# Kernel optimization log

Measured on AMD Instinct MI355X. Metric: run time of the kernel, lower is better.

## Reference

```python
import jax, jax.numpy as jnp
import numpy as np

NUM_GROUPS = 32
NUM_HEADS = 8
EPS = 1e-5


def setup_inputs() -> dict:
    key = jax.random.key(0)
    ks = jax.random.split(key, 3)
    C = 512
    x = jax.random.normal(ks[0], (4, C, 48, 48), dtype=jnp.float32)
    gamma = jnp.ones((C,), jnp.float32)
    beta = jnp.zeros((C,), jnp.float32)
    w_qkv = jax.random.normal(ks[1], (C, 3 * C), jnp.float32) * (1.0 / np.sqrt(C))
    b_qkv = jnp.zeros((3 * C,), jnp.float32)
    w_proj = jax.random.normal(ks[2], (C, C), jnp.float32) * (1.0 / np.sqrt(C))
    b_proj = jnp.zeros((C,), jnp.float32)
    return {"x": x, "gamma": gamma, "beta": beta, "w_qkv": w_qkv,
            "b_qkv": b_qkv, "w_proj": w_proj, "b_proj": b_proj}


def group_norm(x, gamma, beta):
    # x: (b, c, h, w); 32 groups over channel dim
    b, c, h, w = x.shape
    xg = x.reshape(b, NUM_GROUPS, c // NUM_GROUPS, h, w)
    mu = jnp.mean(xg, axis=(2, 3, 4), keepdims=True)
    var = jnp.var(xg, axis=(2, 3, 4), keepdims=True)
    xn = ((xg - mu) * jax.lax.rsqrt(var + EPS)).reshape(b, c, h, w)
    return xn * gamma[None, :, None, None] + beta[None, :, None, None]


def reference(x, gamma, beta, w_qkv, b_qkv, w_proj, b_proj):
    b, c, h, w = x.shape
    hd = c // NUM_HEADS
    scale = hd ** -0.5
    xn = group_norm(x, gamma, beta)
    x_flat = xn.reshape(b, c, h * w).transpose(0, 2, 1)          # (b, s, c)
    qkv = x_flat @ w_qkv + b_qkv                                  # (b, s, 3c)
    q, k, v = jnp.split(qkv, 3, axis=-1)
    s = h * w
    # (b, heads, s, hd)
    q = q.reshape(b, s, NUM_HEADS, hd).transpose(0, 2, 1, 3)
    k = k.reshape(b, s, NUM_HEADS, hd).transpose(0, 2, 1, 3)
    v = v.reshape(b, s, NUM_HEADS, hd).transpose(0, 2, 1, 3)
    attn = jnp.einsum('bhqd,bhkd->bhqk', q, k) * scale            # (b, h, s, s)
    attn = jax.nn.softmax(attn, axis=-1)
    out = jnp.einsum('bhqk,bhkd->bhqd', attn, v)                  # (b, h, s, hd)
    out = out.transpose(0, 2, 1, 3).reshape(b, s, c)
    out = out @ w_proj + b_proj                                   # (b, s, c)
    return x + out.transpose(0, 2, 1).reshape(b, c, h, w)
```

## Files before the change

kernel.cpp:

```cpp
#include <hip/hip_runtime.h>
#include <hip/hip_bf16.h>
#include <stdint.h>

#define S_LEN 2304
#define C_DIM 512
#define NH 8
#define HD 64

typedef __attribute__((ext_vector_type(8))) __bf16 bf16x8;
typedef __attribute__((ext_vector_type(4))) float f32x4;
typedef __attribute__((ext_vector_type(16))) float f32x16;
typedef __attribute__((ext_vector_type(8))) unsigned short u16x8;
typedef __attribute__((ext_vector_type(4))) unsigned short u16x4;

__device__ __forceinline__ unsigned short bf16u(float f) {
  __hip_bfloat16 h = __float2bfloat16(f);
  return __builtin_bit_cast(unsigned short, h);
}

__device__ __forceinline__ void load_lds16(const void* g, void* l) {
  __builtin_amdgcn_global_load_lds(
      (const __attribute__((address_space(1))) void*)g,
      (__attribute__((address_space(3))) void*)l, 16, 0, 0);
}

__global__ __launch_bounds__(256) void gn_stats_kernel(const float* __restrict__ x,
                                                       float* __restrict__ stats) {
  const int bg = blockIdx.x;
  const float4* src = (const float4*)(x + (size_t)bg * 36864);
  float s = 0.f, s2 = 0.f;
#pragma unroll
  for (int i = 0; i < 36; ++i) {
    float4 v = src[i * 256 + threadIdx.x];
    s += v.x + v.y + v.z + v.w;
    s2 += v.x * v.x + v.y * v.y + v.z * v.z + v.w * v.w;
  }
#pragma unroll
  for (int off = 1; off < 64; off <<= 1) {
    s += __shfl_xor(s, off);
    s2 += __shfl_xor(s2, off);
  }
  __shared__ float red[8];
  const int wid = threadIdx.x >> 6;
  if ((threadIdx.x & 63) == 0) { red[wid] = s; red[wid + 4] = s2; }
  __syncthreads();
  if (threadIdx.x == 0) {
    float S = red[0] + red[1] + red[2] + red[3];
    float S2 = red[4] + red[5] + red[6] + red[7];
    float mu = S * (1.f / 36864.f);
    float var = S2 * (1.f / 36864.f) - mu * mu;
    stats[bg * 2] = mu;
    stats[bg * 2 + 1] = rsqrtf(var + 1e-5f);
  }
}

__global__ __launch_bounds__(256) void gn_norm_t_kernel(
    const float* __restrict__ x, const float* __restrict__ gamma,
    const float* __restrict__ beta, const float* __restrict__ stats,
    unsigned short* __restrict__ xn) {
  __shared__ float tile[64][68];
  const int s0 = blockIdx.x * 64, c0 = blockIdx.y * 64, b = blockIdx.z;
  const int tid = threadIdx.x;
  {
    const int cl = tid >> 2, sc = (tid & 3) * 16;
    const float* src = x + ((size_t)b * C_DIM + c0 + cl) * S_LEN + s0 + sc;
#pragma unroll
    for (int i = 0; i < 4; ++i)
      *(float4*)&tile[cl][sc + i * 4] = *(const float4*)(src + i * 4);
  }
  __syncthreads();
  const int sl = tid >> 2, cc = (tid & 3) * 16;
  const int g = (c0 + cc) >> 4;
  const float mu = stats[((size_t)b * 32 + g) * 2];
  const float rs = stats[((size_t)b * 32 + g) * 2 + 1];
  u16x8 o0, o1;
#pragma unroll
  for (int j = 0; j < 8; ++j) {
    const int c = c0 + cc + j;
    o0[j] = bf16u((tile[cc + j][sl] - mu) * rs * gamma[c] + beta[c]);
  }
#pragma unroll
  for (int j = 0; j < 8; ++j) {
    const int c = c0 + cc + 8 + j;
    o1[j] = bf16u((tile[cc + 8 + j][sl] - mu) * rs * gamma[c] + beta[c]);
  }
  unsigned short* dst = xn + ((size_t)b * S_LEN + s0 + sl) * C_DIM + c0 + cc;
  *(u16x8*)dst = o0;
  *(u16x8*)(dst + 8) = o1;
}

__global__ __launch_bounds__(256) void wt_kernel(const float* __restrict__ w,
                                                 unsigned short* __restrict__ wT,
                                                 int N, int K) {
  __shared__ float tile[64][68];
  const int n0 = blockIdx.x * 64, k0 = blockIdx.y * 64;
  const int tid = threadIdx.x;
  {
    const int kl = tid >> 2, nc = (tid & 3) * 16;
    const float* src = w + (size_t)(k0 + kl) * N + n0 + nc;
#pragma unroll
    for (int i = 0; i < 4; ++i)
      *(float4*)&tile[kl][nc + i * 4] = *(const float4*)(src + i * 4);
  }
  __syncthreads();
  const int nl = tid >> 2, kc = (tid & 3) * 16;
  u16x8 o0, o1;
#pragma unroll
  for (int j = 0; j < 8; ++j) o0[j] = bf16u(tile[kc + j][nl]);
#pragma unroll
  for (int j = 0; j < 8; ++j) o1[j] = bf16u(tile[kc + 8 + j][nl]);
  unsigned short* dst = wT + (size_t)(n0 + nl) * K + k0 + kc;
  *(u16x8*)dst = o0;
  *(u16x8*)(dst + 8) = o1;
}

__device__ __forceinline__ void gemm128_core(const unsigned short* __restrict__ A,
                                             const unsigned short* __restrict__ B,
                                             int K, int m0, int n0, short* lds_a,
                                             short* lds_b, f32x4 (&acc)[4][4]) {
  const int tid = threadIdx.x;
  const int lane = tid & 63, wid = tid >> 6;
  const int wr = wid >> 1, wc = wid & 1;
  const f32x4 fzero = {0.f, 0.f, 0.f, 0.f};
#pragma unroll
  for (int i = 0; i < 4; ++i)
#pragma unroll
    for (int j = 0; j < 4; ++j) acc[i][j] = fzero;
  const int lrow = lane >> 3;
  const int lcol = (lane & 7) * 8;
  for (int kt = 0; kt < K; kt += 64) {
#pragma unroll
    for (int i = 0; i < 4; ++i) {
      const int r0 = (wid * 4 + i) * 8;
      load_lds16((const void*)(A + (size_t)(m0 + r0 + lrow) * K + kt + lcol), lds_a + r0 * 64);
      load_lds16((const void*)(B + (size_t)(n0 + r0 + lrow) * K + kt + lcol), lds_b + r0 * 64);
    }
    __syncthreads();
#pragma unroll
    for (int ks = 0; ks < 2; ++ks) {
      bf16x8 af[4], bfr[4];
#pragma unroll
      for (int mf = 0; mf < 4; ++mf)
        af[mf] = *(const bf16x8*)(lds_a + ((wr * 64 + mf * 16 + (lane & 15)) * 64 +
                                           ks * 32 + (lane >> 4) * 8));
#pragma unroll
      for (int nf = 0; nf < 4; ++nf)
        bfr[nf] = *(const bf16x8*)(lds_b + ((wc * 64 + nf * 16 + (lane & 15)) * 64 +
                                            ks * 32 + (lane >> 4) * 8));
#pragma unroll
      for (int mf = 0; mf < 4; ++mf)
#pragma unroll
        for (int nf = 0; nf < 4; ++nf)
          acc[mf][nf] =
              __builtin_amdgcn_mfma_f32_16x16x32_bf16(af[mf], bfr[nf], acc[mf][nf], 0, 0, 0);
    }
    __syncthreads();
  }
}

__global__ __launch_bounds__(256) void qkv_gemm_kernel(
    const unsigned short* __restrict__ xn, const unsigned short* __restrict__ wT,
    const float* __restrict__ bq, unsigned short* __restrict__ Qb,
    unsigned short* __restrict__ Kb, unsigned short* __restrict__ Vt) {
  __shared__ short lds_a[128 * 64];
  __shared__ short lds_b[128 * 64];
  const int b = blockIdx.z;
  const int m0 = blockIdx.x * 128, n0 = blockIdx.y * 128;
  f32x4 acc[4][4];
  gemm128_core(xn + (size_t)b * S_LEN * C_DIM, wT, C_DIM, m0, n0, lds_a, lds_b, acc);
  const int lane = threadIdx.x & 63, wid = threadIdx.x >> 6;
  const int wr = wid >> 1, wc = wid & 1;
#pragma unroll
  for (int mf = 0; mf < 4; ++mf) {
#pragma unroll
    for (int nf = 0; nf < 4; ++nf) {
      const int n = n0 + wc * 64 + nf * 16 + (lane & 15);
      const int part = n >> 9;
      const int h = (n >> 6) & 7;
      const int d = n & 63;
      const float bias = bq[n];
      const int m = m0 + wr * 64 + mf * 16 + (lane >> 4) * 4;
      if (part == 2) {
        u16x4 pk;
#pragma unroll
        for (int r = 0; r < 4; ++r) pk[r] = bf16u(acc[mf][nf][r] + bias);
        *(u16x4*)(Vt + ((size_t)(b * NH + h) * HD + d) * S_LEN + m) = pk;
      } else {
        unsigned short* dst = part == 0 ? Qb : Kb;
        const float sc = part == 0 ? 0.18033688011112042f : 1.0f;
#pragma unroll
        for (int r = 0; r < 4; ++r)
          dst[((size_t)(b * NH + h) * S_LEN + m + r) * HD + d] =
              bf16u((acc[mf][nf][r] + bias) * sc);
      }
    }
  }
}

#define QBLK 96
__global__ __launch_bounds__(192) void attn_kernel(const unsigned short* __restrict__ Q,
                                                   const unsigned short* __restrict__ K,
                                                   const unsigned short* __restrict__ Vt,
                                                   unsigned short* __restrict__ O) {
  __shared__ __align__(16) char smem[45056];
  const int tid = threadIdx.x;
  const int w = tid >> 6, l = tid & 63;
  const int l31 = l & 31, hi = l >> 5;
  const int bh = blockIdx.y, b = bh >> 3, h = bh & 7;
  const int q0 = blockIdx.x * QBLK;

  const char* gQ = (const char*)Q + (size_t)bh * S_LEN * 128;
  const char* gK = (const char*)K + (size_t)bh * S_LEN * 128;
  const char* gV = (const char*)Vt + (size_t)bh * HD * (S_LEN * 2);

  const char* kvp[6];
  unsigned kvadv[6];
  bool kvok[6];
#pragma unroll
  for (int i = 0; i < 6; ++i) {
    const int c = i * 192 + tid;
    kvok[i] = (c < 1024);
    if (c < 512) {
      const int r = c >> 3, ch = c & 7;
      kvp[i] = gK + (size_t)r * 128 + ((ch ^ (r & 7)) << 4);
      kvadv[i] = 64 * 128;
    } else {
      const int c2 = c & 511;
      const int dd = c2 >> 3, ch = c2 & 7;
      kvp[i] = gV + (size_t)dd * (S_LEN * 2) + ((ch ^ (dd & 7)) << 4);
      kvadv[i] = 128;
    }
  }

  auto stage_kv = [&](char* nreg) {
#pragma unroll
    for (int i = 0; i < 6; ++i) {
      if (kvok[i]) {
        load_lds16((const void*)kvp[i], nreg + (i * 192 + w * 64) * 16);
        kvp[i] += kvadv[i];
      }
    }
  };

#pragma unroll
  for (int i = 0; i < 4; ++i) {
    const int c0 = i * 192 + w * 64;
    const int c = c0 + l;
    const int r = c >> 3, ch = c & 7;
    load_lds16((const void*)(gQ + (size_t)(q0 + r) * 128 + ((ch ^ (r & 7)) << 4)),
               smem + c0 * 16);
  }
  stage_kv(smem + 12288);
  if (w == 0) asm volatile("s_waitcnt vmcnt(6)" ::: "memory");
  else        asm volatile("s_waitcnt vmcnt(5)" ::: "memory");
  __builtin_amdgcn_s_barrier();

  bf16x8 qf[4];
  {
    const int qrow = w * 32 + l31;
    const int qsw = qrow & 7;
#pragma unroll
    for (int d4 = 0; d4 < 4; ++d4)
      qf[d4] = *(const bf16x8*)(smem + qrow * 128 + (((d4 * 2 + hi) ^ qsw) << 4));
  }

  float m_run = -1e30f, lsum = 0.f;
  f32x16 oac0, oac1;
#pragma unroll
  for (int i = 0; i < 16; ++i) { oac0[i] = 0.f; oac1[i] = 0.f; }

  for (int kt = 0; kt < 36; ++kt) {
    char* region = smem + 12288 + ((kt & 1) << 14);
    if (kt < 35) {
      stage_kv(smem + 12288 + (((kt + 1) & 1) << 14));
      if (w == 0) asm volatile("s_waitcnt vmcnt(6)" ::: "memory");
      else        asm volatile("s_waitcnt vmcnt(5)" ::: "memory");
    } else {
      asm volatile("s_waitcnt vmcnt(0)" ::: "memory");
    }
    __builtin_amdgcn_s_barrier();

    const char* kreg = region;
    const char* vreg = region + 8192;
#pragma unroll
    for (int sub = 0; sub < 2; ++sub) {
      f32x16 st;
#pragma unroll
      for (int i = 0; i < 16; ++i) st[i] = 0.f;
      const int krow = sub * 32 + l31;
      const int ksw = krow & 7;
#pragma unroll
      for (int d4 = 0; d4 < 4; ++d4) {
        bf16x8 kf = *(const bf16x8*)(kreg + krow * 128 + (((d4 * 2 + hi) ^ ksw) << 4));
        st = __builtin_amdgcn_mfma_f32_32x32x16_bf16(kf, qf[d4], st, 0, 0, 0);
      }
      float t8[8];
#pragma unroll
      for (int i = 0; i < 8; ++i) t8[i] = fmaxf(st[2 * i], st[2 * i + 1]);
#pragma unroll
      for (int i = 0; i < 4; ++i) t8[i] = fmaxf(t8[i], t8[i + 4]);
      float mt = fmaxf(fmaxf(t8[0], t8[1]), fmaxf(t8[2], t8[3]));
      float mo = mt;
      asm volatile("v_permlane32_swap_b32 %0, %1" : "+v"(mt), "+v"(mo));
      mt = fmaxf(mt, mo);
      const float mnew = fmaxf(m_run, mt);
      if (__any((mt - m_run) > 8.f)) {
        const float corr = exp2f(m_run - mnew);
#pragma unroll
        for (int i = 0; i < 16; ++i) { oac0[i] *= corr; oac1[i] *= corr; }
        lsum *= corr;
        m_run = mnew;
      }
      float p[16];
#pragma unroll
      for (int i = 0; i < 16; ++i) p[i] = exp2f(st[i] - m_run);
      float a8[8];
#pragma unroll
      for (int i = 0; i < 8; ++i) a8[i] = p[2 * i] + p[2 * i + 1];
#pragma unroll
      for (int i = 0; i < 4; ++i) a8[i] += a8[i + 4];
      float rs = (a8[0] + a8[1]) + (a8[2] + a8[3]);
      float rsc = rs;
      asm volatile("v_permlane32_swap_b32 %0, %1" : "+v"(rs), "+v"(rsc));
      lsum += rs + rsc;
      unsigned int wv[8];
#pragma unroll
      for (int j = 0; j < 8; ++j)
        asm("v_cvt_pk_bf16_f32 %0, %1, %2" : "=v"(wv[j]) : "v"(p[2 * j]), "v"(p[2 * j + 1]));
      asm volatile("v_permlane32_swap_b32 %0, %1" : "+v"(wv[0]), "+v"(wv[2]));
      asm volatile("v_permlane32_swap_b32 %0, %1" : "+v"(wv[1]), "+v"(wv[3]));
      asm volatile("v_permlane32_swap_b32 %0, %1" : "+v"(wv[4]), "+v"(wv[6]));
      asm volatile("v_permlane32_swap_b32 %0, %1" : "+v"(wv[5]), "+v"(wv[7]));
      typedef __attribute__((ext_vector_type(4))) unsigned int u32x4;
      u32x4 pw0 = {wv[0], wv[1], wv[2], wv[3]};
      u32x4 pw1 = {wv[4], wv[5], wv[6], wv[7]};
      bf16x8 pf0 = __builtin_bit_cast(bf16x8, pw0);
      bf16x8 pf1 = __builtin_bit_cast(bf16x8, pw1);
      {
        const int vrow = l31;
        const int vsw = vrow & 7;
        bf16x8 vf0 = *(const bf16x8*)(vreg + vrow * 128 + (((sub * 4 + 0 + hi) ^ vsw) << 4));
        oac0 = __builtin_amdgcn_mfma_f32_32x32x16_bf16(vf0, pf0, oac0, 0, 0, 0);
        bf16x8 vf1 = *(const bf16x8*)(vreg + vrow * 128 + (((sub * 4 + 2 + hi) ^ vsw) << 4));
        oac0 = __builtin_amdgcn_mfma_f32_32x32x16_bf16(vf1, pf1, oac0, 0, 0, 0);
      }
      {
        const int vrow = 32 + l31;
        const int vsw = vrow & 7;
        bf16x8 vf0 = *(const bf16x8*)(vreg + vrow * 128 + (((sub * 4 + 0 + hi) ^ vsw) << 4));
        oac1 = __builtin_amdgcn_mfma_f32_32x32x16_bf16(vf0, pf0, oac1, 0, 0, 0);
        bf16x8 vf1 = *(const bf16x8*)(vreg + vrow * 128 + (((sub * 4 + 2 + hi) ^ vsw) << 4));
        oac1 = __builtin_amdgcn_mfma_f32_32x32x16_bf16(vf1, pf1, oac1, 0, 0, 0);
      }
    }
    __builtin_amdgcn_s_barrier();
  }

  __syncthreads();
  const float inv = 1.f / lsum;
  unsigned short* ob = (unsigned short*)smem;
  const int qrow = w * 32 + l31;
#pragma unroll
  for (int g = 0; g < 4; ++g) {
    u16x4 pk;
#pragma unroll
    for (int r = 0; r < 4; ++r) pk[r] = bf16u(oac0[g * 4 + r] * inv);
    *(u16x4*)(ob + qrow * 72 + (g * 8 + hi * 4)) = pk;
  }
#pragma unroll
  for (int g = 0; g < 4; ++g) {
    u16x4 pk;
#pragma unroll
    for (int r = 0; r < 4; ++r) pk[r] = bf16u(oac1[g * 4 + r] * inv);
    *(u16x4*)(ob + qrow * 72 + (32 + g * 8 + hi * 4)) = pk;
  }
  __syncthreads();
#pragma unroll
  for (int i = 0; i < 4; ++i) {
    const int c = i * 192 + tid;
    const int row = c >> 3, c8 = (c & 7) * 8;
    u16x8 v = *(const u16x8*)(ob + row * 72 + c8);
    *(u16x8*)(O + ((size_t)b * S_LEN + q0 + row) * C_DIM + h * HD + c8) = v;
  }
}

__global__ __launch_bounds__(256) void proj_gemm_kernel(
    const unsigned short* __restrict__ wT, const unsigned short* __restrict__ ao,
    const float* __restrict__ bp, const float* __restrict__ x, float* __restrict__ out) {
  __shared__ short lds_a[128 * 64];
  __shared__ short lds_b[128 * 64];
  const int b = blockIdx.z;
  const int m0 = blockIdx.x * 128, n0 = blockIdx.y * 128;
  f32x4 acc[4][4];
  gemm128_core(wT, ao + (size_t)b * S_LEN * C_DIM, C_DIM, m0, n0, lds_a, lds_b, acc);
  const int lane = threadIdx.x & 63, wid = threadIdx.x >> 6;
  const int wr = wid >> 1, wc = wid & 1;
#pragma unroll
  for (int mf = 0; mf < 4; ++mf) {
#pragma unroll
    for (int nf = 0; nf < 4; ++nf) {
      const int n = n0 + wc * 64 + nf * 16 + (lane & 15);
#pragma unroll
      for (int r = 0; r < 4; ++r) {
        const int m = m0 + wr * 64 + mf * 16 + (lane >> 4) * 4 + r;
        const size_t idx = ((size_t)b * C_DIM + m) * S_LEN + n;
        out[idx] = x[idx] + acc[mf][nf][r] + bp[m];
      }
    }
  }
}

extern "C" void kernel_launch(void* const* d_in, const int* in_sizes, int n_in,
                              void* d_out, int out_size, void* d_ws, size_t ws_size,
                              hipStream_t stream) {
  const float* x = (const float*)d_in[0];
  const float* gamma = (const float*)d_in[1];
  const float* beta = (const float*)d_in[2];
  const float* w_qkv = (const float*)d_in[3];
  const float* b_qkv = (const float*)d_in[4];
  const float* w_proj = (const float*)d_in[5];
  const float* b_proj = (const float*)d_in[6];
  float* out = (float*)d_out;

  char* ws = (char*)d_ws;
  float* stats = (float*)ws;
  unsigned short* xn = (unsigned short*)(ws + 1024);
  unsigned short* wqkvT = (unsigned short*)(ws + 9438208);
  unsigned short* wprojT = (unsigned short*)(ws + 11011072);
  unsigned short* Qb = (unsigned short*)(ws + 11535360);
  unsigned short* Kb = (unsigned short*)(ws + 20972544);
  unsigned short* Vt = (unsigned short*)(ws + 30409728);
  unsigned short* ao = (unsigned short*)(ws + 39846912);

  hipLaunchKernelGGL(gn_stats_kernel, dim3(128), dim3(256), 0, stream, x, stats);
  hipLaunchKernelGGL(wt_kernel, dim3(24, 8), dim3(256), 0, stream, w_qkv, wqkvT, 3 * C_DIM, C_DIM);
  hipLaunchKernelGGL(wt_kernel, dim3(8, 8), dim3(256), 0, stream, w_proj, wprojT, C_DIM, C_DIM);
  hipLaunchKernelGGL(gn_norm_t_kernel, dim3(36, 8, 4), dim3(256), 0, stream, x, gamma, beta, stats, xn);
  hipLaunchKernelGGL(qkv_gemm_kernel, dim3(18, 12, 4), dim3(256), 0, stream, xn, wqkvT, b_qkv, Qb, Kb, Vt);
  hipLaunchKernelGGL(attn_kernel, dim3(24, 32), dim3(192), 0, stream, Qb, Kb, Vt, ao);
  hipLaunchKernelGGL(proj_gemm_kernel, dim3(4, 18, 4), dim3(256), 0, stream, wprojT, ao, b_proj, x, out);
}
```

Baseline: 179.3 us.

## Triple-buffer K/V staging, load Q to registers, compute row sums with MFMA

New measurement: 194.3 us. 8.4% more time.

```diff
diff --git a/kernel.cpp b/kernel.cpp
--- a/kernel.cpp
+++ b/kernel.cpp
@@ -12,6 +12,7 @@
 typedef __attribute__((ext_vector_type(16))) float f32x16;
 typedef __attribute__((ext_vector_type(8))) unsigned short u16x8;
 typedef __attribute__((ext_vector_type(4))) unsigned short u16x4;
+typedef __attribute__((ext_vector_type(4))) unsigned int u32x4;
 
 __device__ __forceinline__ unsigned short bf16u(float f) {
   __hip_bfloat16 h = __float2bfloat16(f);
@@ -22,6 +23,12 @@
   __builtin_amdgcn_global_load_lds(
       (const __attribute__((address_space(1))) void*)g,
       (__attribute__((address_space(3))) void*)l, 16, 0, 0);
+}
+
+__device__ __forceinline__ float max3f(float a, float b, float c) {
+  float d;
+  asm("v_max3_f32 %0, %1, %2, %3" : "=v"(d) : "v"(a), "v"(b), "v"(c));
+  return d;
 }
 
 __global__ __launch_bounds__(256) void gn_stats_kernel(const float* __restrict__ x,
@@ -202,7 +209,7 @@
                                                    const unsigned short* __restrict__ K,
                                                    const unsigned short* __restrict__ Vt,
                                                    unsigned short* __restrict__ O) {
-  __shared__ __align__(16) char smem[45056];
+  __shared__ __align__(16) char smem[49152];
   const int tid = threadIdx.x;
   const int w = tid >> 6, l = tid & 63;
   const int l31 = l & 31, hi = l >> 5;
@@ -212,6 +219,14 @@
   const char* gQ = (const char*)Q + (size_t)bh * S_LEN * 128;
   const char* gK = (const char*)K + (size_t)bh * S_LEN * 128;
   const char* gV = (const char*)Vt + (size_t)bh * HD * (S_LEN * 2);
+
+  bf16x8 qf[4];
+  {
+    const char* qp = gQ + (size_t)(q0 + w * 32 + l31) * 128 + hi * 16;
+#pragma unroll
+    for (int d4 = 0; d4 < 4; ++d4) qf[d4] = *(const bf16x8*)(qp + d4 * 32);
+  }
+  asm volatile("" : "+v"(qf[0]), "+v"(qf[1]), "+v"(qf[2]), "+v"(qf[3]));
 
   const char* kvp[6];
   unsigned kvadv[6];
@@ -242,37 +257,26 @@
     }
   };
 
-#pragma unroll
-  for (int i = 0; i < 4; ++i) {
-    const int c0 = i * 192 + w * 64;
-    const int c = c0 + l;
-    const int r = c >> 3, ch = c & 7;
-    load_lds16((const void*)(gQ + (size_t)(q0 + r) * 128 + ((ch ^ (r & 7)) << 4)),
-               smem + c0 * 16);
-  }
-  stage_kv(smem + 12288);
-  if (w == 0) asm volatile("s_waitcnt vmcnt(6)" ::: "memory");
-  else        asm volatile("s_waitcnt vmcnt(5)" ::: "memory");
-  __builtin_amdgcn_s_barrier();
-
-  bf16x8 qf[4];
-  {
-    const int qrow = w * 32 + l31;
-    const int qsw = qrow & 7;
-#pragma unroll
-    for (int d4 = 0; d4 < 4; ++d4)
-      qf[d4] = *(const bf16x8*)(smem + qrow * 128 + (((d4 * 2 + hi) ^ qsw) << 4));
-  }
-
-  float m_run = -1e30f, lsum = 0.f;
-  f32x16 oac0, oac1;
-#pragma unroll
-  for (int i = 0; i < 16; ++i) { oac0[i] = 0.f; oac1[i] = 0.f; }
-
+  stage_kv(smem);
+  stage_kv(smem + 16384);
+
+  const u16x8 onesu = {0x3F80, 0x3F80, 0x3F80, 0x3F80, 0x3F80, 0x3F80, 0x3F80, 0x3F80};
+  const bf16x8 onesf = __builtin_bit_cast(bf16x8, onesu);
+
+  float m_run = -1e30f;
+  f32x16 oac0, oac1, lacc;
+#pragma unroll
+  for (int i = 0; i < 16; ++i) { oac0[i] = 0.f; oac1[i] = 0.f; lacc[i] = 0.f; }
+
+  int cur = 0;
   for (int kt = 0; kt < 36; ++kt) {
-    char* region = smem + 12288 + ((kt & 1) << 14);
-    if (kt < 35) {
-      stage_kv(smem + 12288 + (((kt + 1) & 1) << 14));
+    char* region = smem + cur * 16384;
+    if (kt <= 33) {
+      int nxt = cur + 2; if (nxt >= 3) nxt -= 3;
+      stage_kv(smem + nxt * 16384);
+      if (w == 0) asm volatile("s_waitcnt vmcnt(12)" ::: "memory");
+      else        asm volatile("s_waitcnt vmcnt(10)" ::: "memory");
+    } else if (kt == 34) {
       if (w == 0) asm volatile("s_waitcnt vmcnt(6)" ::: "memory");
       else        asm volatile("s_waitcnt vmcnt(5)" ::: "memory");
     } else {
@@ -294,35 +298,29 @@
         bf16x8 kf = *(const bf16x8*)(kreg + krow * 128 + (((d4 * 2 + hi) ^ ksw) << 4));
         st = __builtin_amdgcn_mfma_f32_32x32x16_bf16(kf, qf[d4], st, 0, 0, 0);
       }
-      float t8[8];
-#pragma unroll
-      for (int i = 0; i < 8; ++i) t8[i] = fmaxf(st[2 * i], st[2 * i + 1]);
-#pragma unroll
-      for (int i = 0; i < 4; ++i) t8[i] = fmaxf(t8[i], t8[i + 4]);
-      float mt = fmaxf(fmaxf(t8[0], t8[1]), fmaxf(t8[2], t8[3]));
-      float mo = mt;
-      asm volatile("v_permlane32_swap_b32 %0, %1" : "+v"(mt), "+v"(mo));
-      mt = fmaxf(mt, mo);
-      const float mnew = fmaxf(m_run, mt);
+      float m0 = max3f(st[0], st[1], st[2]);
+      float m1 = max3f(st[3], st[4], st[5]);
+      float m2 = max3f(st[6], st[7], st[8]);
+      float m3 = max3f(st[9], st[10], st[11]);
+      float m4 = max3f(st[12], st[13], st[14]);
+      float mt = max3f(m0, m1, st[15]);
+      float mb = max3f(m2, m3, m4);
+      mt = fmaxf(mt, mb);
+      {
+        float mo = mt;
+        asm volatile("v_permlane32_swap_b32 %0, %1" : "+v"(mt), "+v"(mo));
+        mt = fmaxf(mt, mo);
+      }
       if (__any((mt - m_run) > 8.f)) {
+        const float mnew = fmaxf(m_run, mt);
         const float corr = exp2f(m_run - mnew);
 #pragma unroll
-        for (int i = 0; i < 16; ++i) { oac0[i] *= corr; oac1[i] *= corr; }
-        lsum *= corr;
+        for (int i = 0; i < 16; ++i) { oac0[i] *= corr; oac1[i] *= corr; lacc[i] *= corr; }
         m_run = mnew;
       }
       float p[16];
 #pragma unroll
       for (int i = 0; i < 16; ++i) p[i] = exp2f(st[i] - m_run);
-      float a8[8];
-#pragma unroll
-      for (int i = 0; i < 8; ++i) a8[i] = p[2 * i] + p[2 * i + 1];
-#pragma unroll
-      for (int i = 0; i < 4; ++i) a8[i] += a8[i + 4];
-      float rs = (a8[0] + a8[1]) + (a8[2] + a8[3]);
-      float rsc = rs;
-      asm volatile("v_permlane32_swap_b32 %0, %1" : "+v"(rs), "+v"(rsc));
-      lsum += rs + rsc;
       unsigned int wv[8];
 #pragma unroll
       for (int j = 0; j < 8; ++j)
@@ -331,11 +329,12 @@
       asm volatile("v_permlane32_swap_b32 %0, %1" : "+v"(wv[1]), "+v"(wv[3]));
       asm volatile("v_permlane32_swap_b32 %0, %1" : "+v"(wv[4]), "+v"(wv[6]));
       asm volatile("v_permlane32_swap_b32 %0, %1" : "+v"(wv[5]), "+v"(wv[7]));
-      typedef __attribute__((ext_vector_type(4))) unsigned int u32x4;
       u32x4 pw0 = {wv[0], wv[1], wv[2], wv[3]};
       u32x4 pw1 = {wv[4], wv[5], wv[6], wv[7]};
       bf16x8 pf0 = __builtin_bit_cast(bf16x8, pw0);
       bf16x8 pf1 = __builtin_bit_cast(bf16x8, pw1);
+      lacc = __builtin_amdgcn_mfma_f32_32x32x16_bf16(onesf, pf0, lacc, 0, 0, 0);
+      lacc = __builtin_amdgcn_mfma_f32_32x32x16_bf16(onesf, pf1, lacc, 0, 0, 0);
       {
         const int vrow = l31;
         const int vsw = vrow & 7;
@@ -354,10 +353,11 @@
       }
     }
     __builtin_amdgcn_s_barrier();
+    ++cur; if (cur >= 3) cur -= 3;
   }
 
   __syncthreads();
-  const float inv = 1.f / lsum;
+  const float inv = 1.f / lacc[0];
   unsigned short* ob = (unsigned short*)smem;
   const int qrow = w * 32 + l31;
 #pragma unroll
```

## Remap attention blocks per XCD and issue both QK^T tiles before softmax

Applied to the files above, without the earlier changes.

Result: slower. 192.3 us (+7.2%).

```diff
diff --git a/kernel.cpp b/kernel.cpp
--- a/kernel.cpp
+++ b/kernel.cpp
@@ -12,6 +12,7 @@
 typedef __attribute__((ext_vector_type(16))) float f32x16;
 typedef __attribute__((ext_vector_type(8))) unsigned short u16x8;
 typedef __attribute__((ext_vector_type(4))) unsigned short u16x4;
+typedef __attribute__((ext_vector_type(4))) unsigned int u32x4;
 
 __device__ __forceinline__ unsigned short bf16u(float f) {
   __hip_bfloat16 h = __float2bfloat16(f);
@@ -206,8 +207,12 @@
   const int tid = threadIdx.x;
   const int w = tid >> 6, l = tid & 63;
   const int l31 = l & 31, hi = l >> 5;
-  const int bh = blockIdx.y, b = bh >> 3, h = bh & 7;
-  const int q0 = blockIdx.x * QBLK;
+  const int L = blockIdx.y * 24 + blockIdx.x;
+  const int xcd = L & 7, j = L >> 3;
+  const int bh = xcd * 4 + j / 24;
+  const int qt = j % 24;
+  const int b = bh >> 3, h = bh & 7;
+  const int q0 = qt * QBLK;
 
   const char* gQ = (const char*)Q + (size_t)bh * S_LEN * 128;
   const char* gK = (const char*)K + (size_t)bh * S_LEN * 128;
@@ -282,29 +287,39 @@
 
     const char* kreg = region;
     const char* vreg = region + 8192;
-#pragma unroll
-    for (int sub = 0; sub < 2; ++sub) {
-      f32x16 st;
-#pragma unroll
-      for (int i = 0; i < 16; ++i) st[i] = 0.f;
-      const int krow = sub * 32 + l31;
-      const int ksw = krow & 7;
+
+    f32x16 st0, st1;
+#pragma unroll
+    for (int i = 0; i < 16; ++i) { st0[i] = 0.f; st1[i] = 0.f; }
+    {
+      const int kr0 = l31, sw0 = kr0 & 7;
 #pragma unroll
       for (int d4 = 0; d4 < 4; ++d4) {
-        bf16x8 kf = *(const bf16x8*)(kreg + krow * 128 + (((d4 * 2 + hi) ^ ksw) << 4));
-        st = __builtin_amdgcn_mfma_f32_32x32x16_bf16(kf, qf[d4], st, 0, 0, 0);
-      }
+        bf16x8 kf = *(const bf16x8*)(kreg + kr0 * 128 + (((d4 * 2 + hi) ^ sw0) << 4));
+        st0 = __builtin_amdgcn_mfma_f32_32x32x16_bf16(kf, qf[d4], st0, 0, 0, 0);
+      }
+      const int kr1 = 32 + l31, sw1 = kr1 & 7;
+#pragma unroll
+      for (int d4 = 0; d4 < 4; ++d4) {
+        bf16x8 kf = *(const bf16x8*)(kreg + kr1 * 128 + (((d4 * 2 + hi) ^ sw1) << 4));
+        st1 = __builtin_amdgcn_mfma_f32_32x32x16_bf16(kf, qf[d4], st1, 0, 0, 0);
+      }
+    }
+
+    auto smpv = [&](f32x16& st, int sub) {
       float t8[8];
 #pragma unroll
       for (int i = 0; i < 8; ++i) t8[i] = fmaxf(st[2 * i], st[2 * i + 1]);
 #pragma unroll
       for (int i = 0; i < 4; ++i) t8[i] = fmaxf(t8[i], t8[i + 4]);
       float mt = fmaxf(fmaxf(t8[0], t8[1]), fmaxf(t8[2], t8[3]));
-      float mo = mt;
-      asm volatile("v_permlane32_swap_b32 %0, %1" : "+v"(mt), "+v"(mo));
-      mt = fmaxf(mt, mo);
-      const float mnew = fmaxf(m_run, mt);
+      {
+        float mo = mt;
+        asm volatile("v_permlane32_swap_b32 %0, %1" : "+v"(mt), "+v"(mo));
+        mt = fmaxf(mt, mo);
+      }
       if (__any((mt - m_run) > 8.f)) {
+        const float mnew = fmaxf(m_run, mt);
         const float corr = exp2f(m_run - mnew);
 #pragma unroll
         for (int i = 0; i < 16; ++i) { oac0[i] *= corr; oac1[i] *= corr; }
@@ -325,13 +340,12 @@
       lsum += rs + rsc;
       unsigned int wv[8];
 #pragma unroll
-      for (int j = 0; j < 8; ++j)
-        asm("v_cvt_pk_bf16_f32 %0, %1, %2" : "=v"(wv[j]) : "v"(p[2 * j]), "v"(p[2 * j + 1]));
+      for (int jj = 0; jj < 8; ++jj)
+        asm("v_cvt_pk_bf16_f32 %0, %1, %2" : "=v"(wv[jj]) : "v"(p[2 * jj]), "v"(p[2 * jj + 1]));
       asm volatile("v_permlane32_swap_b32 %0, %1" : "+v"(wv[0]), "+v"(wv[2]));
       asm volatile("v_permlane32_swap_b32 %0, %1" : "+v"(wv[1]), "+v"(wv[3]));
       asm volatile("v_permlane32_swap_b32 %0, %1" : "+v"(wv[4]), "+v"(wv[6]));
       asm volatile("v_permlane32_swap_b32 %0, %1" : "+v"(wv[5]), "+v"(wv[7]));
-      typedef __attribute__((ext_vector_type(4))) unsigned int u32x4;
       u32x4 pw0 = {wv[0], wv[1], wv[2], wv[3]};
       u32x4 pw1 = {wv[4], wv[5], wv[6], wv[7]};
       bf16x8 pf0 = __builtin_bit_cast(bf16x8, pw0);
@@ -352,7 +366,10 @@
         bf16x8 vf1 = *(const bf16x8*)(vreg + vrow * 128 + (((sub * 4 + 2 + hi) ^ vsw) << 4));
         oac1 = __builtin_amdgcn_mfma_f32_32x32x16_bf16(vf1, pf1, oac1, 0, 0, 0);
       }
-    }
+    };
+    smpv(st0, 0);
+    smpv(st1, 1);
+
     __builtin_amdgcn_s_barrier();
   }
 
```

## Split attention KV range across wave pairs with XCD-aware block mapping

Applied to the files above, without the earlier changes.

After: 162.9 us. -9.1%, faster.

```diff
diff --git a/kernel.cpp b/kernel.cpp
--- a/kernel.cpp
+++ b/kernel.cpp
@@ -12,6 +12,7 @@
 typedef __attribute__((ext_vector_type(16))) float f32x16;
 typedef __attribute__((ext_vector_type(8))) unsigned short u16x8;
 typedef __attribute__((ext_vector_type(4))) unsigned short u16x4;
+typedef __attribute__((ext_vector_type(4))) unsigned int u32x4;
 
 __device__ __forceinline__ unsigned short bf16u(float f) {
   __hip_bfloat16 h = __float2bfloat16(f);
@@ -197,72 +198,62 @@
   }
 }
 
-#define QBLK 96
-__global__ __launch_bounds__(192) void attn_kernel(const unsigned short* __restrict__ Q,
-                                                   const unsigned short* __restrict__ K,
-                                                   const unsigned short* __restrict__ Vt,
-                                                   unsigned short* __restrict__ O) {
-  __shared__ __align__(16) char smem[45056];
+#define QBLK 64
+__global__ __launch_bounds__(256, 4) void attn_kernel(const unsigned short* __restrict__ Q,
+                                                      const unsigned short* __restrict__ K,
+                                                      const unsigned short* __restrict__ Vt,
+                                                      unsigned short* __restrict__ O) {
+  __shared__ __align__(16) char smem[32768];
   const int tid = threadIdx.x;
   const int w = tid >> 6, l = tid & 63;
   const int l31 = l & 31, hi = l >> 5;
-  const int bh = blockIdx.y, b = bh >> 3, h = bh & 7;
-  const int q0 = blockIdx.x * QBLK;
+  const int ks = w & 1, qw = w >> 1;
+  const int L = blockIdx.y * 36 + blockIdx.x;
+  const int xcd = L & 7, j = L >> 3;
+  const int bh = xcd * 4 + j / 36;
+  const int qt = j % 36;
+  const int b = bh >> 3, h = bh & 7;
+  const int q0 = qt * QBLK;
 
   const char* gQ = (const char*)Q + (size_t)bh * S_LEN * 128;
   const char* gK = (const char*)K + (size_t)bh * S_LEN * 128;
   const char* gV = (const char*)Vt + (size_t)bh * HD * (S_LEN * 2);
 
-  const char* kvp[6];
-  unsigned kvadv[6];
-  bool kvok[6];
-#pragma unroll
-  for (int i = 0; i < 6; ++i) {
-    const int c = i * 192 + tid;
-    kvok[i] = (c < 1024);
-    if (c < 512) {
-      const int r = c >> 3, ch = c & 7;
-      kvp[i] = gK + (size_t)r * 128 + ((ch ^ (r & 7)) << 4);
-      kvadv[i] = 64 * 128;
-    } else {
-      const int c2 = c & 511;
-      const int dd = c2 >> 3, ch = c2 & 7;
-      kvp[i] = gV + (size_t)dd * (S_LEN * 2) + ((ch ^ (dd & 7)) << 4);
-      kvadv[i] = 128;
-    }
-  }
-
-  auto stage_kv = [&](char* nreg) {
-#pragma unroll
-    for (int i = 0; i < 6; ++i) {
-      if (kvok[i]) {
-        load_lds16((const void*)kvp[i], nreg + (i * 192 + w * 64) * 16);
-        kvp[i] += kvadv[i];
-      }
-    }
-  };
-
-#pragma unroll
-  for (int i = 0; i < 4; ++i) {
-    const int c0 = i * 192 + w * 64;
-    const int c = c0 + l;
-    const int r = c >> 3, ch = c & 7;
-    load_lds16((const void*)(gQ + (size_t)(q0 + r) * 128 + ((ch ^ (r & 7)) << 4)),
-               smem + c0 * 16);
-  }
-  stage_kv(smem + 12288);
-  if (w == 0) asm volatile("s_waitcnt vmcnt(6)" ::: "memory");
-  else        asm volatile("s_waitcnt vmcnt(5)" ::: "memory");
-  __builtin_amdgcn_s_barrier();
-
   bf16x8 qf[4];
   {
-    const int qrow = w * 32 + l31;
-    const int qsw = qrow & 7;
-#pragma unroll
-    for (int d4 = 0; d4 < 4; ++d4)
-      qf[d4] = *(const bf16x8*)(smem + qrow * 128 + (((d4 * 2 + hi) ^ qsw) << 4));
-  }
+    const char* qp = gQ + (size_t)(q0 + qw * 32 + l31) * 128 + hi * 16;
+#pragma unroll
+    for (int d4 = 0; d4 < 4; ++d4) qf[d4] = *(const bf16x8*)(qp + d4 * 32);
+  }
+
+  const int sr = tid >> 3, sch = tid & 7;
+  const char* pk0;
+  const char* pv0;
+  {
+    pk0 = gK + (size_t)sr * 128 + ((sch ^ (sr & 7)) << 4);
+    const int co = sch ^ (sr & 7);
+    const int vd = 2 * sr + (co >> 2), slot = co & 3;
+    pv0 = gV + (size_t)vd * (S_LEN * 2) + slot * 16;
+  }
+  const char* pk1 = pk0 + 1152 * 128;
+  const char* pv1 = pv0 + 1152 * 2;
+
+  auto stage = [&](int dbuf) {
+    char* base = smem + dbuf * 8192 + tid * 16;
+    load_lds16((const void*)pk0, base);
+    load_lds16((const void*)pv0, base + 4096);
+    load_lds16((const void*)pk1, base + 16384);
+    load_lds16((const void*)pv1, base + 16384 + 4096);
+    pk0 += 4096; pv0 += 64; pk1 += 4096; pv1 += 64;
+  };
+
+  stage(0);
+
+  const u16x8 onesu = {0x3F80, 0x3F80, 0x3F80, 0x3F80, 0x3F80, 0x3F80, 0x3F80, 0x3F80};
+  const bf16x8 onesf = __builtin_bit_cast(bf16x8, onesu);
+  f32x16 z16;
+#pragma unroll
+  for (int i = 0; i < 16; ++i) z16[i] = 0.f;
 
   float m_run = -1e30f, lsum = 0.f;
   f32x16 oac0, oac1;
@@ -270,117 +261,138 @@
   for (int i = 0; i < 16; ++i) { oac0[i] = 0.f; oac1[i] = 0.f; }
 
   for (int kt = 0; kt < 36; ++kt) {
-    char* region = smem + 12288 + ((kt & 1) << 14);
     if (kt < 35) {
-      stage_kv(smem + 12288 + (((kt + 1) & 1) << 14));
-      if (w == 0) asm volatile("s_waitcnt vmcnt(6)" ::: "memory");
-      else        asm volatile("s_waitcnt vmcnt(5)" ::: "memory");
+      stage((kt + 1) & 1);
+      asm volatile("s_waitcnt vmcnt(4)" ::: "memory");
     } else {
       asm volatile("s_waitcnt vmcnt(0)" ::: "memory");
     }
     __builtin_amdgcn_s_barrier();
 
-    const char* kreg = region;
-    const char* vreg = region + 8192;
-#pragma unroll
-    for (int sub = 0; sub < 2; ++sub) {
-      f32x16 st;
-#pragma unroll
-      for (int i = 0; i < 16; ++i) st[i] = 0.f;
-      const int krow = sub * 32 + l31;
-      const int ksw = krow & 7;
+    const char* kreg = smem + ks * 16384 + (kt & 1) * 8192;
+    const char* vreg = kreg + 4096;
+
+    f32x16 st;
+#pragma unroll
+    for (int i = 0; i < 16; ++i) st[i] = 0.f;
+    {
+      const int ksw = l31 & 7;
 #pragma unroll
       for (int d4 = 0; d4 < 4; ++d4) {
-        bf16x8 kf = *(const bf16x8*)(kreg + krow * 128 + (((d4 * 2 + hi) ^ ksw) << 4));
+        bf16x8 kf = *(const bf16x8*)(kreg + l31 * 128 + (((d4 * 2 + hi) ^ ksw) << 4));
         st = __builtin_amdgcn_mfma_f32_32x32x16_bf16(kf, qf[d4], st, 0, 0, 0);
       }
-      float t8[8];
-#pragma unroll
-      for (int i = 0; i < 8; ++i) t8[i] = fmaxf(st[2 * i], st[2 * i + 1]);
-#pragma unroll
-      for (int i = 0; i < 4; ++i) t8[i] = fmaxf(t8[i], t8[i + 4]);
-      float mt = fmaxf(fmaxf(t8[0], t8[1]), fmaxf(t8[2], t8[3]));
+    }
+    float t8[8];
+#pragma unroll
+    for (int i = 0; i < 8; ++i) t8[i] = fmaxf(st[2 * i], st[2 * i + 1]);
+#pragma unroll
+    for (int i = 0; i < 4; ++i) t8[i] = fmaxf(t8[i], t8[i + 4]);
+    float mt = fmaxf(fmaxf(t8[0], t8[1]), fmaxf(t8[2], t8[3]));
+    {
       float mo = mt;
       asm volatile("v_permlane32_swap_b32 %0, %1" : "+v"(mt), "+v"(mo));
       mt = fmaxf(mt, mo);
+    }
+    if (__any((mt - m_run) > 8.f)) {
       const float mnew = fmaxf(m_run, mt);
-      if (__any((mt - m_run) > 8.f)) {
-        const float corr = exp2f(m_run - mnew);
-#pragma unroll
-        for (int i = 0; i < 16; ++i) { oac0[i] *= corr; oac1[i] *= corr; }
-        lsum *= corr;
-        m_run = mnew;
-      }
-      float p[16];
-#pragma unroll
-      for (int i = 0; i < 16; ++i) p[i] = exp2f(st[i] - m_run);
-      float a8[8];
-#pragma unroll
-      for (int i = 0; i < 8; ++i) a8[i] = p[2 * i] + p[2 * i + 1];
-#pragma unroll
-      for (int i = 0; i < 4; ++i) a8[i] += a8[i + 4];
-      float rs = (a8[0] + a8[1]) + (a8[2] + a8[3]);
-      float rsc = rs;
-      asm volatile("v_permlane32_swap_b32 %0, %1" : "+v"(rs), "+v"(rsc));
-      lsum += rs + rsc;
-      unsigned int wv[8];
-#pragma unroll
-      for (int j = 0; j < 8; ++j)
-        asm("v_cvt_pk_bf16_f32 %0, %1, %2" : "=v"(wv[j]) : "v"(p[2 * j]), "v"(p[2 * j + 1]));
-      asm volatile("v_permlane32_swap_b32 %0, %1" : "+v"(wv[0]), "+v"(wv[2]));
-      asm volatile("v_permlane32_swap_b32 %0, %1" : "+v"(wv[1]), "+v"(wv[3]));
-      asm volatile("v_permlane32_swap_b32 %0, %1" : "+v"(wv[4]), "+v"(wv[6]));
-      asm volatile("v_permlane32_swap_b32 %0, %1" : "+v"(wv[5]), "+v"(wv[7]));
-      typedef __attribute__((ext_vector_type(4))) unsigned int u32x4;
-      u32x4 pw0 = {wv[0], wv[1], wv[2], wv[3]};
-      u32x4 pw1 = {wv[4], wv[5], wv[6], wv[7]};
-      bf16x8 pf0 = __builtin_bit_cast(bf16x8, pw0);
-      bf16x8 pf1 = __builtin_bit_cast(bf16x8, pw1);
-      {
-        const int vrow = l31;
-        const int vsw = vrow & 7;
-        bf16x8 vf0 = *(const bf16x8*)(vreg + vrow * 128 + (((sub * 4 + 0 + hi) ^ vsw) << 4));
-        oac0 = __builtin_amdgcn_mfma_f32_32x32x16_bf16(vf0, pf0, oac0, 0, 0, 0);
-        bf16x8 vf1 = *(const bf16x8*)(vreg + vrow * 128 + (((sub * 4 + 2 + hi) ^ vsw) << 4));
-        oac0 = __builtin_amdgcn_mfma_f32_32x32x16_bf16(vf1, pf1, oac0, 0, 0, 0);
-      }
-      {
-        const int vrow = 32 + l31;
-        const int vsw = vrow & 7;
-        bf16x8 vf0 = *(const bf16x8*)(vreg + vrow * 128 + (((sub * 4 + 0 + hi) ^ vsw) << 4));
-        oac1 = __builtin_amdgcn_mfma_f32_32x32x16_bf16(vf0, pf0, oac1, 0, 0, 0);
-        bf16x8 vf1 = *(const bf16x8*)(vreg + vrow * 128 + (((sub * 4 + 2 + hi) ^ vsw) << 4));
-        oac1 = __builtin_amdgcn_mfma_f32_32x32x16_bf16(vf1, pf1, oac1, 0, 0, 0);
-      }
+      const float corr = exp2f(m_run - mnew);
+#pragma unroll
+      for (int i = 0; i < 16; ++i) { oac0[i] *= corr; oac1[i] *= corr; }
+      lsum *= corr;
+      m_run = mnew;
+    }
+    float p[16];
+#pragma unroll
+    for (int i = 0; i < 16; ++i) p[i] = exp2f(st[i] - m_run);
+    unsigned int wv[8];
+#pragma unroll
+    for (int jj = 0; jj < 8; ++jj)
+      asm("v_cvt_pk_bf16_f32 %0, %1, %2" : "=v"(wv[jj]) : "v"(p[2 * jj]), "v"(p[2 * jj + 1]));
+    asm volatile("v_permlane32_swap_b32 %0, %1" : "+v"(wv[0]), "+v"(wv[2]));
+    asm volatile("v_permlane32_swap_b32 %0, %1" : "+v"(wv[1]), "+v"(wv[3]));
+    asm volatile("v_permlane32_swap_b32 %0, %1" : "+v"(wv[4]), "+v"(wv[6]));
+    asm volatile("v_permlane32_swap_b32 %0, %1" : "+v"(wv[5]), "+v"(wv[7]));
+    u32x4 pw0 = {wv[0], wv[1], wv[2], wv[3]};
+    u32x4 pw1 = {wv[4], wv[5], wv[6], wv[7]};
+    bf16x8 pf0 = __builtin_bit_cast(bf16x8, pw0);
+    bf16x8 pf1 = __builtin_bit_cast(bf16x8, pw1);
+    {
+      f32x16 tmp = __builtin_amdgcn_mfma_f32_32x32x16_bf16(onesf, pf0, z16, 0, 0, 0);
+      tmp = __builtin_amdgcn_mfma_f32_32x32x16_bf16(onesf, pf1, tmp, 0, 0, 0);
+      lsum += tmp[0];
+    }
+    {
+      const int vr = l31 >> 1;
+      const int c0 = ((l31 & 1) * 4 + hi) ^ (vr & 7);
+      const int c1 = ((l31 & 1) * 4 + 2 + hi) ^ (vr & 7);
+      bf16x8 vf0 = *(const bf16x8*)(vreg + vr * 128 + (c0 << 4));
+      oac0 = __builtin_amdgcn_mfma_f32_32x32x16_bf16(vf0, pf0, oac0, 0, 0, 0);
+      bf16x8 vf1 = *(const bf16x8*)(vreg + vr * 128 + (c1 << 4));
+      oac0 = __builtin_amdgcn_mfma_f32_32x32x16_bf16(vf1, pf1, oac0, 0, 0, 0);
+    }
+    {
+      const int vr = 16 + (l31 >> 1);
+      const int c0 = ((l31 & 1) * 4 + hi) ^ (vr & 7);
+      const int c1 = ((l31 & 1) * 4 + 2 + hi) ^ (vr & 7);
+      bf16x8 vf0 = *(const bf16x8*)(vreg + vr * 128 + (c0 << 4));
+      oac1 = __builtin_amdgcn_mfma_f32_32x32x16_bf16(vf0, pf0, oac1, 0, 0, 0);
+      bf16x8 vf1 = *(const bf16x8*)(vreg + vr * 128 + (c1 << 4));
+      oac1 = __builtin_amdgcn_mfma_f32_32x32x16_bf16(vf1, pf1, oac1, 0, 0, 0);
     }
     __builtin_amdgcn_s_barrier();
   }
 
   __syncthreads();
-  const float inv = 1.f / lsum;
-  unsigned short* ob = (unsigned short*)smem;
-  const int qrow = w * 32 + l31;
-#pragma unroll
-  for (int g = 0; g < 4; ++g) {
-    u16x4 pk;
-#pragma unroll
-    for (int r = 0; r < 4; ++r) pk[r] = bf16u(oac0[g * 4 + r] * inv);
-    *(u16x4*)(ob + qrow * 72 + (g * 8 + hi * 4)) = pk;
-  }
-#pragma unroll
-  for (int g = 0; g < 4; ++g) {
-    u16x4 pk;
-#pragma unroll
-    for (int r = 0; r < 4; ++r) pk[r] = bf16u(oac1[g * 4 + r] * inv);
-    *(u16x4*)(ob + qrow * 72 + (32 + g * 8 + hi * 4)) = pk;
-  }
-  __syncthreads();
-#pragma unroll
-  for (int i = 0; i < 4; ++i) {
-    const int c = i * 192 + tid;
-    const int row = c >> 3, c8 = (c & 7) * 8;
-    u16x8 v = *(const u16x8*)(ob + row * 72 + c8);
-    *(u16x8*)(O + ((size_t)b * S_LEN + q0 + row) * C_DIM + h * HD + c8) = v;
+  float* fl = (float*)smem;
+  float* obuf = fl + 512;
+  if (hi == 0) {
+    fl[w * 32 + l31] = m_run;
+    fl[128 + w * 32 + l31] = lsum;
+  }
+  __syncthreads();
+  const float pm = fl[(w ^ 1) * 32 + l31];
+  const float pl = fl[128 + (w ^ 1) * 32 + l31];
+  const float mM = fmaxf(m_run, pm);
+  const float sOwn = exp2f(m_run - mM);
+  const float newl = lsum * sOwn + pl * exp2f(pm - mM);
+  const int q = qw * 32 + l31;
+  if (ks == 0) {
+    if (hi == 0) fl[256 + q] = 1.f / newl;
+#pragma unroll
+    for (int g = 0; g < 4; ++g) {
+      float4 v0 = {oac0[g * 4] * sOwn, oac0[g * 4 + 1] * sOwn, oac0[g * 4 + 2] * sOwn,
+                   oac0[g * 4 + 3] * sOwn};
+      *(float4*)&obuf[q * 68 + g * 8 + hi * 4] = v0;
+      float4 v1 = {oac1[g * 4] * sOwn, oac1[g * 4 + 1] * sOwn, oac1[g * 4 + 2] * sOwn,
+                   oac1[g * 4 + 3] * sOwn};
+      *(float4*)&obuf[q * 68 + 32 + g * 8 + hi * 4] = v1;
+    }
+  }
+  __syncthreads();
+  if (ks == 1) {
+#pragma unroll
+    for (int g = 0; g < 4; ++g) {
+      float4 v0 = *(const float4*)&obuf[q * 68 + g * 8 + hi * 4];
+      v0.x += oac0[g * 4] * sOwn; v0.y += oac0[g * 4 + 1] * sOwn;
+      v0.z += oac0[g * 4 + 2] * sOwn; v0.w += oac0[g * 4 + 3] * sOwn;
+      *(float4*)&obuf[q * 68 + g * 8 + hi * 4] = v0;
+      float4 v1 = *(const float4*)&obuf[q * 68 + 32 + g * 8 + hi * 4];
+      v1.x += oac1[g * 4] * sOwn; v1.y += oac1[g * 4 + 1] * sOwn;
+      v1.z += oac1[g * 4 + 2] * sOwn; v1.w += oac1[g * 4 + 3] * sOwn;
+      *(float4*)&obuf[q * 68 + 32 + g * 8 + hi * 4] = v1;
+    }
+  }
+  __syncthreads();
+#pragma unroll
+  for (int i = 0; i < 2; ++i) {
+    const int c = i * 256 + tid;
+    const int r = c >> 3, ch = c & 7;
+    const float invr = fl[256 + r];
+    u16x8 o;
+#pragma unroll
+    for (int jj = 0; jj < 8; ++jj) o[jj] = bf16u(obuf[r * 68 + ch * 8 + jj] * invr);
+    *(u16x8*)(O + ((size_t)b * S_LEN + q0 + r) * C_DIM + h * HD + ch * 8) = o;
   }
 }
 
@@ -437,6 +449,6 @@
   hipLaunchKernelGGL(wt_kernel, dim3(8, 8), dim3(256), 0, stream, w_proj, wprojT, C_DIM, C_DIM);
   hipLaunchKernelGGL(gn_norm_t_kernel, dim3(36, 8, 4), dim3(256), 0, stream, x, gamma, beta, stats, xn);
   hipLaunchKernelGGL(qkv_gemm_kernel, dim3(18, 12, 4), dim3(256), 0, stream, xn, wqkvT, b_qkv, Qb, Kb, Vt);
-  hipLaunchKernelGGL(attn_kernel, dim3(24, 32), dim3(192), 0, stream, Qb, Kb, Vt, ao);
+  hipLaunchKernelGGL(attn_kernel, dim3(36, 32), dim3(256), 0, stream, Qb, Kb, Vt, ao);
   hipLaunchKernelGGL(proj_gemm_kernel, dim3(4, 18, 4), dim3(256), 0, stream, wprojT, ao, b_proj, x, out);
 }
```
